# Kernel optimization log

Measured on AMD Instinct MI355X. Metric: run time of the kernel, lower is better.

## Reference

```python
import jax, jax.numpy as jnp
import numpy as np

NUM_NODES = 262144
NUM_GRAPHS = 256
D_MODEL = 256
LOG_2 = float(np.log(2.0))


def setup_inputs() -> dict:
    key = jax.random.key(0)
    k1, k2, k3 = jax.random.split(key, 3)
    l_enc = jax.random.normal(k1, (NUM_NODES, D_MODEL), dtype=jnp.float32)
    g_enc = jax.random.normal(k2, (NUM_GRAPHS, D_MODEL), dtype=jnp.float32)
    batch = jax.random.randint(k3, (NUM_NODES,), 0, NUM_GRAPHS, dtype=jnp.int64)
    return {"l_enc": l_enc, "g_enc": g_enc, "batch": batch}


def reference(l_enc, g_enc, batch):
    # local_global_loss_ with measure='JSD', mask=[] (msk == ones)
    num_nodes = l_enc.shape[0]
    num_graphs = g_enc.shape[0]
    # pos_mask: one-hot of graph id per node; neg_mask is its complement
    pos_mask = jax.nn.one_hot(batch, num_graphs, dtype=l_enc.dtype)  # [N, G]
    neg_mask = 1.0 - pos_mask
    res = jnp.einsum('nd,gd->ng', l_enc, g_enc)                      # [N, G]
    # JSD positive expectation on res*pos_mask (zeros contribute 0)
    Ep = LOG_2 - jax.nn.softplus(-(res * pos_mask))
    # JSD negative expectation on res*neg_mask (zeros contribute 0)
    rq = res * neg_mask
    Eq = jax.nn.softplus(-rq) + rq - LOG_2
    E_pos = jnp.sum(Ep) / num_nodes
    E_neg = jnp.sum(Eq) / (num_nodes * (num_graphs - 1))
    return E_neg - E_pos
```

## Files before the change

### kernel.cpp

```cpp
#include <hip/hip_runtime.h>
#include <hip/hip_bf16.h>

#define N_NODES 262144
#define N_GRAPHS 256
#define DMODEL 256
#define LN2 0.6931471805599453094

typedef __attribute__((ext_vector_type(4))) float f32x4;
typedef __attribute__((ext_vector_type(8))) short short8;

__device__ __forceinline__ short bf(float x) {
    __hip_bfloat16 h = __float2bfloat16(x);
    return __builtin_bit_cast(short, h);
}

__device__ __forceinline__ short8 cvt8(f32x4 lo, f32x4 hi) {
    short8 a;
    a[0] = bf(lo[0]); a[1] = bf(lo[1]); a[2] = bf(lo[2]); a[3] = bf(lo[3]);
    a[4] = bf(hi[0]); a[5] = bf(hi[1]); a[6] = bf(hi[2]); a[7] = bf(hi[3]);
    return a;
}

__device__ __forceinline__ void mfma8(short8 a, const char* bb, f32x4* acc) {
#pragma unroll
    for (int nt = 0; nt < 8; ++nt) {
        short8 bfrag = *reinterpret_cast<const short8*>(bb + nt * 1024);
        acc[nt] = __builtin_amdgcn_mfma_f32_16x16x32_bf16(a, bfrag, acc[nt], 0, 0, 0);
    }
}

__device__ __forceinline__ void elem(float r, int col, int bv,
                                     float& Sl2, float& Sl2p, float& Spr) {
    float t = fminf(r, 64.f) * 1.44269504f;
    float l2 = __log2f(1.f + exp2f(t));
    Sl2 += l2;
    float m = (col == bv) ? 1.f : 0.f;
    Sl2p = fmaf(m, l2, Sl2p);
    Spr = fmaf(m, r, Spr);
}

__global__ __launch_bounds__(256, 1) void mvgrl_main(
    const float* __restrict__ l_enc, const float* __restrict__ g_enc,
    const int* __restrict__ batch, double* __restrict__ partials) {
    extern __shared__ char lds_raw[];

    const int tid = threadIdx.x;
    const int lane = tid & 63;
    const int wave = tid >> 6;
    const int bid = blockIdx.x;

    const int rg = (bid >> 4) * 8 + (bid & 7);
    const int chalf = (bid >> 3) & 1;
    const int row_blk = rg * 1024;
    const int kofs = (lane >> 4) * 8;

    f32x4 s0l, s0h, s1l, s1h, s2l, s2h, s3l, s3h;
    const float* arow = l_enc +
        (size_t)(row_blk + wave * 16 + (lane & 15)) * DMODEL + kofs;
    s0l = *reinterpret_cast<const f32x4*>(arow + 0);
    s0h = *reinterpret_cast<const f32x4*>(arow + 4);
    s1l = *reinterpret_cast<const f32x4*>(arow + 32);
    s1h = *reinterpret_cast<const f32x4*>(arow + 36);
    s2l = *reinterpret_cast<const f32x4*>(arow + 64);
    s2h = *reinterpret_cast<const f32x4*>(arow + 68);
    s3l = *reinterpret_cast<const f32x4*>(arow + 96);
    s3h = *reinterpret_cast<const f32x4*>(arow + 100);

    {
        short8* lb = reinterpret_cast<short8*>(lds_raw);
#pragma unroll 2
        for (int i = 0; i < 16; ++i) {
            int c = wave + i * 4;
            int nt = c & 7, ks = c >> 3;
            int g = chalf * 128 + nt * 16 + (lane & 15);
            int k = ks * 32 + (lane >> 4) * 8;
            const float* src = g_enc + g * DMODEL + k;
            f32x4 lo = *reinterpret_cast<const f32x4*>(src);
            f32x4 hi = *reinterpret_cast<const f32x4*>(src + 4);
            lb[c * 64 + lane] = cvt8(lo, hi);
        }
    }
    __syncthreads();

    const char* ldsB = lds_raw + lane * 16;
    double dS0 = 0.0, dS1 = 0.0, dS2 = 0.0;

#pragma unroll 1
    for (int pass = 0; pass < 16; ++pass) {
        const int rowbase = row_blk + pass * 64 + wave * 16;
        const int rsub = (lane >> 4) * 4;
        int bv0 = batch[rowbase + rsub + 0];
        int bv1 = batch[rowbase + rsub + 1];
        int bv2 = batch[rowbase + rsub + 2];
        int bv3 = batch[rowbase + rsub + 3];

        const float* arow_next = l_enc +
            (size_t)(row_blk + ((pass + 1) & 15) * 64 + wave * 16 + (lane & 15)) *
                DMODEL + kofs;

        f32x4 acc[8];
#pragma unroll
        for (int n = 0; n < 8; ++n) acc[n] = (f32x4){0.f, 0.f, 0.f, 0.f};

#pragma unroll 1
        for (int g = 0; g < 2; ++g) {
            const float* src = (g == 0) ? (arow + 128) : arow_next;
            const char* lb = ldsB + (size_t)g * 4 * 8192;
            {
                short8 a = cvt8(s0l, s0h);
                s0l = *reinterpret_cast<const f32x4*>(src + 0);
                s0h = *reinterpret_cast<const f32x4*>(src + 4);
                mfma8(a, lb + 0 * 8192, acc);
            }
            {
                short8 a = cvt8(s1l, s1h);
                s1l = *reinterpret_cast<const f32x4*>(src + 32);
                s1h = *reinterpret_cast<const f32x4*>(src + 36);
                mfma8(a, lb + 1 * 8192, acc);
            }
            {
                short8 a = cvt8(s2l, s2h);
                s2l = *reinterpret_cast<const f32x4*>(src + 64);
                s2h = *reinterpret_cast<const f32x4*>(src + 68);
                mfma8(a, lb + 2 * 8192, acc);
            }
            {
                short8 a = cvt8(s3l, s3h);
                s3l = *reinterpret_cast<const f32x4*>(src + 96);
                s3h = *reinterpret_cast<const f32x4*>(src + 100);
                mfma8(a, lb + 3 * 8192, acc);
            }
        }
        arow = arow_next;

        float Sl2 = 0.f, Sl2p = 0.f, Spr = 0.f;
        const int colbase = chalf * 128 + (lane & 15);
#pragma unroll
        for (int nt = 0; nt < 8; ++nt) {
            const int col = colbase + nt * 16;
            f32x4 av = acc[nt];
            elem(av[0], col, bv0, Sl2, Sl2p, Spr);
            elem(av[1], col, bv1, Sl2, Sl2p, Spr);
            elem(av[2], col, bv2, Sl2, Sl2p, Spr);
            elem(av[3], col, bv3, Sl2, Sl2p, Spr);
        }
        dS0 += (double)Sl2;
        dS1 += (double)Sl2p;
        dS2 += (double)Spr;
    }

#pragma unroll
    for (int off = 32; off; off >>= 1) {
        dS0 += __shfl_xor(dS0, off);
        dS1 += __shfl_xor(dS1, off);
        dS2 += __shfl_xor(dS2, off);
    }
    __syncthreads();
    double* red = reinterpret_cast<double*>(lds_raw);
    if (lane == 0) {
        red[wave * 3 + 0] = dS0;
        red[wave * 3 + 1] = dS1;
        red[wave * 3 + 2] = dS2;
    }
    __syncthreads();
    if (tid == 0) {
        double a = 0, b = 0, c = 0;
#pragma unroll
        for (int w = 0; w < 4; ++w) {
            a += red[w * 3 + 0];
            b += red[w * 3 + 1];
            c += red[w * 3 + 2];
        }
        partials[bid * 3 + 0] = a;
        partials[bid * 3 + 1] = b;
        partials[bid * 3 + 2] = c;
    }
}

__global__ void finalize_kernel(const double* __restrict__ p,
                                float* __restrict__ out) {
    int t = threadIdx.x;
    double a = p[t * 3 + 0], b = p[t * 3 + 1], c = p[t * 3 + 2];
#pragma unroll
    for (int off = 32; off; off >>= 1) {
        a += __shfl_xor(a, off);
        b += __shfl_xor(b, off);
        c += __shfl_xor(c, off);
    }
    __shared__ double red[24];
    int lane = t & 63, w = t >> 6;
    if (lane == 0) { red[w * 3] = a; red[w * 3 + 1] = b; red[w * 3 + 2] = c; }
    __syncthreads();
    if (t == 0) {
        double A = 0, B = 0, C = 0;
#pragma unroll
        for (int i = 0; i < 8; ++i) {
            A += red[i * 3]; B += red[i * 3 + 1]; C += red[i * 3 + 2];
        }
        const double NN = (double)N_NODES, GG = (double)N_GRAPHS;
        double Sall_q = LN2 * A - NN * GG * LN2;
        double Spq = LN2 * B - NN * LN2;
        double Spr = C;
        double neg = (Sall_q - Spq) / (NN * (GG - 1.0));
        double pos = (Spr - Spq) / NN;
        out[0] = (float)(neg - pos);
    }
}

extern "C" void kernel_launch(void* const* d_in, const int* in_sizes, int n_in,
                              void* d_out, int out_size, void* d_ws,
                              size_t ws_size, hipStream_t stream) {
    const float* l_enc = (const float*)d_in[0];
    const float* g_enc = (const float*)d_in[1];
    const int* batch = (const int*)d_in[2];
    float* out = (float*)d_out;

    double* partials = (double*)d_ws;

    (void)hipFuncSetAttribute(reinterpret_cast<const void*>(mvgrl_main),
                              hipFuncAttributeMaxDynamicSharedMemorySize, 65536);

    mvgrl_main<<<512, 256, 65536, stream>>>(l_enc, g_enc, batch, partials);
    finalize_kernel<<<1, 512, 0, stream>>>(partials, out);
}
```

Measured before the change: 83.86 us.

## Keep g_enc B fragments in registers and double-buffer l_enc rows in LDS

Each wave now keeps its 64-column slice of g_enc (all 256 K) as bf16 fragments in registers. Each block handles 512 rows across all 256 columns, where before two blocks split the columns of each row group. l_enc rows are staged 16 at a time through a padded, double-buffered LDS tile shared by all four waves, so each row is read from global memory once instead of twice. This costs a block-wide barrier every 16 rows, many more live registers (32 short8 B fragments), and narrower per-wave MFMA work per step.

```diff
diff --git a/kernel.cpp b/kernel.cpp
--- a/kernel.cpp
+++ b/kernel.cpp
@@ -5,6 +5,7 @@
 #define N_GRAPHS 256
 #define DMODEL 256
 #define LN2 0.6931471805599453094
+#define ROW_STRIDE 1040
 
 typedef __attribute__((ext_vector_type(4))) float f32x4;
 typedef __attribute__((ext_vector_type(8))) short short8;
@@ -19,14 +20,6 @@
     a[0] = bf(lo[0]); a[1] = bf(lo[1]); a[2] = bf(lo[2]); a[3] = bf(lo[3]);
     a[4] = bf(hi[0]); a[5] = bf(hi[1]); a[6] = bf(hi[2]); a[7] = bf(hi[3]);
     return a;
-}
-
-__device__ __forceinline__ void mfma8(short8 a, const char* bb, f32x4* acc) {
-#pragma unroll
-    for (int nt = 0; nt < 8; ++nt) {
-        short8 bfrag = *reinterpret_cast<const short8*>(bb + nt * 1024);
-        acc[nt] = __builtin_amdgcn_mfma_f32_16x16x32_bf16(a, bfrag, acc[nt], 0, 0, 0);
-    }
 }
 
 __device__ __forceinline__ void elem(float r, int col, int bv,
@@ -48,105 +41,122 @@
     const int lane = tid & 63;
     const int wave = tid >> 6;
     const int bid = blockIdx.x;
-
-    const int rg = (bid >> 4) * 8 + (bid & 7);
-    const int chalf = (bid >> 3) & 1;
-    const int row_blk = rg * 1024;
-    const int kofs = (lane >> 4) * 8;
-
-    f32x4 s0l, s0h, s1l, s1h, s2l, s2h, s3l, s3h;
-    const float* arow = l_enc +
-        (size_t)(row_blk + wave * 16 + (lane & 15)) * DMODEL + kofs;
-    s0l = *reinterpret_cast<const f32x4*>(arow + 0);
-    s0h = *reinterpret_cast<const f32x4*>(arow + 4);
-    s1l = *reinterpret_cast<const f32x4*>(arow + 32);
-    s1h = *reinterpret_cast<const f32x4*>(arow + 36);
-    s2l = *reinterpret_cast<const f32x4*>(arow + 64);
-    s2h = *reinterpret_cast<const f32x4*>(arow + 68);
-    s3l = *reinterpret_cast<const f32x4*>(arow + 96);
-    s3h = *reinterpret_cast<const f32x4*>(arow + 100);
+    const int row_blk = bid * 512;
+
+    short8 b0_0, b0_1, b0_2, b0_3, b1_0, b1_1, b1_2, b1_3;
+    short8 b2_0, b2_1, b2_2, b2_3, b3_0, b3_1, b3_2, b3_3;
+    short8 b4_0, b4_1, b4_2, b4_3, b5_0, b5_1, b5_2, b5_3;
+    short8 b6_0, b6_1, b6_2, b6_3, b7_0, b7_1, b7_2, b7_3;
+#define LOADB(ks, nt) { \
+    const float* s = g_enc + \
+        (size_t)(wave * 64 + nt * 16 + (lane & 15)) * DMODEL + \
+        ks * 32 + (lane >> 4) * 8; \
+    b##ks##_##nt = cvt8(*reinterpret_cast<const f32x4*>(s), \
+                        *reinterpret_cast<const f32x4*>(s + 4)); }
+    LOADB(0,0) LOADB(0,1) LOADB(0,2) LOADB(0,3)
+    LOADB(1,0) LOADB(1,1) LOADB(1,2) LOADB(1,3)
+    LOADB(2,0) LOADB(2,1) LOADB(2,2) LOADB(2,3)
+    LOADB(3,0) LOADB(3,1) LOADB(3,2) LOADB(3,3)
+    LOADB(4,0) LOADB(4,1) LOADB(4,2) LOADB(4,3)
+    LOADB(5,0) LOADB(5,1) LOADB(5,2) LOADB(5,3)
+    LOADB(6,0) LOADB(6,1) LOADB(6,2) LOADB(6,3)
+    LOADB(7,0) LOADB(7,1) LOADB(7,2) LOADB(7,3)
+#undef LOADB
+
+    char* abuf0 = lds_raw;
+    char* abuf1 = lds_raw + 16 * ROW_STRIDE;
 
     {
-        short8* lb = reinterpret_cast<short8*>(lds_raw);
-#pragma unroll 2
-        for (int i = 0; i < 16; ++i) {
-            int c = wave + i * 4;
-            int nt = c & 7, ks = c >> 3;
-            int g = chalf * 128 + nt * 16 + (lane & 15);
-            int k = ks * 32 + (lane >> 4) * 8;
-            const float* src = g_enc + g * DMODEL + k;
-            f32x4 lo = *reinterpret_cast<const f32x4*>(src);
-            f32x4 hi = *reinterpret_cast<const f32x4*>(src + 4);
-            lb[c * 64 + lane] = cvt8(lo, hi);
-        }
+        const float* g = l_enc + (size_t)(row_blk + wave * 4) * DMODEL;
+        f32x4 t0 = *reinterpret_cast<const f32x4*>(g + 0 * DMODEL + lane * 4);
+        f32x4 t1 = *reinterpret_cast<const f32x4*>(g + 1 * DMODEL + lane * 4);
+        f32x4 t2 = *reinterpret_cast<const f32x4*>(g + 2 * DMODEL + lane * 4);
+        f32x4 t3 = *reinterpret_cast<const f32x4*>(g + 3 * DMODEL + lane * 4);
+        *reinterpret_cast<f32x4*>(abuf0 + (wave * 4 + 0) * ROW_STRIDE + lane * 16) = t0;
+        *reinterpret_cast<f32x4*>(abuf0 + (wave * 4 + 1) * ROW_STRIDE + lane * 16) = t1;
+        *reinterpret_cast<f32x4*>(abuf0 + (wave * 4 + 2) * ROW_STRIDE + lane * 16) = t2;
+        *reinterpret_cast<f32x4*>(abuf0 + (wave * 4 + 3) * ROW_STRIDE + lane * 16) = t3;
     }
     __syncthreads();
 
-    const char* ldsB = lds_raw + lane * 16;
     double dS0 = 0.0, dS1 = 0.0, dS2 = 0.0;
 
 #pragma unroll 1
-    for (int pass = 0; pass < 16; ++pass) {
-        const int rowbase = row_blk + pass * 64 + wave * 16;
+    for (int p = 0; p < 32; ++p) {
+        char* acur = (p & 1) ? abuf1 : abuf0;
+        char* anxt = (p & 1) ? abuf0 : abuf1;
+        const int rowbase = row_blk + p * 16;
+
+        const int pn = (p + 1) & 31;
+        const float* g = l_enc + (size_t)(row_blk + pn * 16 + wave * 4) * DMODEL;
+        f32x4 t0 = *reinterpret_cast<const f32x4*>(g + 0 * DMODEL + lane * 4);
+        f32x4 t1 = *reinterpret_cast<const f32x4*>(g + 1 * DMODEL + lane * 4);
+        f32x4 t2 = *reinterpret_cast<const f32x4*>(g + 2 * DMODEL + lane * 4);
+        f32x4 t3 = *reinterpret_cast<const f32x4*>(g + 3 * DMODEL + lane * 4);
+
         const int rsub = (lane >> 4) * 4;
         int bv0 = batch[rowbase + rsub + 0];
         int bv1 = batch[rowbase + rsub + 1];
         int bv2 = batch[rowbase + rsub + 2];
         int bv3 = batch[rowbase + rsub + 3];
 
-        const float* arow_next = l_enc +
-            (size_t)(row_blk + ((pass + 1) & 15) * 64 + wave * 16 + (lane & 15)) *
-                DMODEL + kofs;
-
-        f32x4 acc[8];
-#pragma unroll
-        for (int n = 0; n < 8; ++n) acc[n] = (f32x4){0.f, 0.f, 0.f, 0.f};
-
-#pragma unroll 1
-        for (int g = 0; g < 2; ++g) {
-            const float* src = (g == 0) ? (arow + 128) : arow_next;
-            const char* lb = ldsB + (size_t)g * 4 * 8192;
-            {
-                short8 a = cvt8(s0l, s0h);
-                s0l = *reinterpret_cast<const f32x4*>(src + 0);
-                s0h = *reinterpret_cast<const f32x4*>(src + 4);
-                mfma8(a, lb + 0 * 8192, acc);
-            }
-            {
-                short8 a = cvt8(s1l, s1h);
-                s1l = *reinterpret_cast<const f32x4*>(src + 32);
-                s1h = *reinterpret_cast<const f32x4*>(src + 36);
-                mfma8(a, lb + 1 * 8192, acc);
-            }
-            {
-                short8 a = cvt8(s2l, s2h);
-                s2l = *reinterpret_cast<const f32x4*>(src + 64);
-                s2h = *reinterpret_cast<const f32x4*>(src + 68);
-                mfma8(a, lb + 2 * 8192, acc);
-            }
-            {
-                short8 a = cvt8(s3l, s3h);
-                s3l = *reinterpret_cast<const f32x4*>(src + 96);
-                s3h = *reinterpret_cast<const f32x4*>(src + 100);
-                mfma8(a, lb + 3 * 8192, acc);
-            }
-        }
-        arow = arow_next;
+        f32x4 acc0 = (f32x4){0.f, 0.f, 0.f, 0.f};
+        f32x4 acc1 = (f32x4){0.f, 0.f, 0.f, 0.f};
+        f32x4 acc2 = (f32x4){0.f, 0.f, 0.f, 0.f};
+        f32x4 acc3 = (f32x4){0.f, 0.f, 0.f, 0.f};
+
+        const char* ar = acur + (lane & 15) * ROW_STRIDE + (lane >> 4) * 32;
+#define KSTEP(ks) { \
+        f32x4 alo = *reinterpret_cast<const f32x4*>(ar + ks * 128); \
+        f32x4 ahi = *reinterpret_cast<const f32x4*>(ar + ks * 128 + 16); \
+        short8 a = cvt8(alo, ahi); \
+        acc0 = __builtin_amdgcn_mfma_f32_16x16x32_bf16(a, b##ks##_0, acc0, 0, 0, 0); \
+        acc1 = __builtin_amdgcn_mfma_f32_16x16x32_bf16(a, b##ks##_1, acc1, 0, 0, 0); \
+        acc2 = __builtin_amdgcn_mfma_f32_16x16x32_bf16(a, b##ks##_2, acc2, 0, 0, 0); \
+        acc3 = __builtin_amdgcn_mfma_f32_16x16x32_bf16(a, b##ks##_3, acc3, 0, 0, 0); }
+        KSTEP(0) KSTEP(1) KSTEP(2) KSTEP(3)
+        KSTEP(4) KSTEP(5) KSTEP(6) KSTEP(7)
+#undef KSTEP
 
         float Sl2 = 0.f, Sl2p = 0.f, Spr = 0.f;
-        const int colbase = chalf * 128 + (lane & 15);
-#pragma unroll
-        for (int nt = 0; nt < 8; ++nt) {
-            const int col = colbase + nt * 16;
-            f32x4 av = acc[nt];
-            elem(av[0], col, bv0, Sl2, Sl2p, Spr);
-            elem(av[1], col, bv1, Sl2, Sl2p, Spr);
-            elem(av[2], col, bv2, Sl2, Sl2p, Spr);
-            elem(av[3], col, bv3, Sl2, Sl2p, Spr);
+        const int colbase = wave * 64 + (lane & 15);
+        {
+            const int col = colbase + 0;
+            elem(acc0[0], col, bv0, Sl2, Sl2p, Spr);
+            elem(acc0[1], col, bv1, Sl2, Sl2p, Spr);
+            elem(acc0[2], col, bv2, Sl2, Sl2p, Spr);
+            elem(acc0[3], col, bv3, Sl2, Sl2p, Spr);
+        }
+        {
+            const int col = colbase + 16;
+            elem(acc1[0], col, bv0, Sl2, Sl2p, Spr);
+            elem(acc1[1], col, bv1, Sl2, Sl2p, Spr);
+            elem(acc1[2], col, bv2, Sl2, Sl2p, Spr);
+            elem(acc1[3], col, bv3, Sl2, Sl2p, Spr);
+        }
+        {
+            const int col = colbase + 32;
+            elem(acc2[0], col, bv0, Sl2, Sl2p, Spr);
+            elem(acc2[1], col, bv1, Sl2, Sl2p, Spr);
+            elem(acc2[2], col, bv2, Sl2, Sl2p, Spr);
+            elem(acc2[3], col, bv3, Sl2, Sl2p, Spr);
+        }
+        {
+            const int col = colbase + 48;
+            elem(acc3[0], col, bv0, Sl2, Sl2p, Spr);
+            elem(acc3[1], col, bv1, Sl2, Sl2p, Spr);
+            elem(acc3[2], col, bv2, Sl2, Sl2p, Spr);
+            elem(acc3[3], col, bv3, Sl2, Sl2p, Spr);
         }
         dS0 += (double)Sl2;
         dS1 += (double)Sl2p;
         dS2 += (double)Spr;
+
+        *reinterpret_cast<f32x4*>(anxt + (wave * 4 + 0) * ROW_STRIDE + lane * 16) = t0;
+        *reinterpret_cast<f32x4*>(anxt + (wave * 4 + 1) * ROW_STRIDE + lane * 16) = t1;
+        *reinterpret_cast<f32x4*>(anxt + (wave * 4 + 2) * ROW_STRIDE + lane * 16) = t2;
+        *reinterpret_cast<f32x4*>(anxt + (wave * 4 + 3) * ROW_STRIDE + lane * 16) = t3;
+        __syncthreads();
     }
 
 #pragma unroll
@@ -155,7 +165,6 @@
         dS1 += __shfl_xor(dS1, off);
         dS2 += __shfl_xor(dS2, off);
     }
-    __syncthreads();
     double* red = reinterpret_cast<double*>(lds_raw);
     if (lane == 0) {
         red[wave * 3 + 0] = dS0;
@@ -218,8 +227,8 @@
     double* partials = (double*)d_ws;
 
     (void)hipFuncSetAttribute(reinterpret_cast<const void*>(mvgrl_main),
-                              hipFuncAttributeMaxDynamicSharedMemorySize, 65536);
-
-    mvgrl_main<<<512, 256, 65536, stream>>>(l_enc, g_enc, batch, partials);
+                              hipFuncAttributeMaxDynamicSharedMemorySize, 33280);
+
+    mvgrl_main<<<512, 256, 33280, stream>>>(l_enc, g_enc, batch, partials);
     finalize_kernel<<<1, 512, 0, stream>>>(partials, out);
 }
```

Measured after the change: 124.7 us. 1.49x slower.

## Switch MFMA tiling from 16x16x32 to 32x32x16 bf16 with 32-row wave tiles

Applied to the files above, without the earlier changes.

Replaces the 16x16x32 bf16 MFMA tiling with 32x32x16 instructions. Each wave now computes a 32x128 tile per pass, so the kernel runs half as many passes. The A-fragment loads, LDS layout of g_enc, batch index gather and epilogue mapping are all reworked to match the 32x32 accumulator layout. The aim is fewer LDS B-fragment reads per FLOP and better MFMA efficiency, at the cost of larger accumulators (64 floats per lane) and more batch loads per lane.

```diff
diff --git a/kernel.cpp b/kernel.cpp
--- a/kernel.cpp
+++ b/kernel.cpp
@@ -7,6 +7,7 @@
 #define LN2 0.6931471805599453094
 
 typedef __attribute__((ext_vector_type(4))) float f32x4;
+typedef __attribute__((ext_vector_type(16))) float f32x16;
 typedef __attribute__((ext_vector_type(8))) short short8;
 
 __device__ __forceinline__ short bf(float x) {
@@ -19,14 +20,6 @@
     a[0] = bf(lo[0]); a[1] = bf(lo[1]); a[2] = bf(lo[2]); a[3] = bf(lo[3]);
     a[4] = bf(hi[0]); a[5] = bf(hi[1]); a[6] = bf(hi[2]); a[7] = bf(hi[3]);
     return a;
-}
-
-__device__ __forceinline__ void mfma8(short8 a, const char* bb, f32x4* acc) {
-#pragma unroll
-    for (int nt = 0; nt < 8; ++nt) {
-        short8 bfrag = *reinterpret_cast<const short8*>(bb + nt * 1024);
-        acc[nt] = __builtin_amdgcn_mfma_f32_16x16x32_bf16(a, bfrag, acc[nt], 0, 0, 0);
-    }
 }
 
 __device__ __forceinline__ void elem(float r, int col, int bv,
@@ -52,28 +45,29 @@
     const int rg = (bid >> 4) * 8 + (bid & 7);
     const int chalf = (bid >> 3) & 1;
     const int row_blk = rg * 1024;
-    const int kofs = (lane >> 4) * 8;
+    const int alane = lane & 31;
+    const int aoct = (lane >> 5) * 8;
 
     f32x4 s0l, s0h, s1l, s1h, s2l, s2h, s3l, s3h;
     const float* arow = l_enc +
-        (size_t)(row_blk + wave * 16 + (lane & 15)) * DMODEL + kofs;
+        (size_t)(row_blk + wave * 32 + alane) * DMODEL + aoct;
     s0l = *reinterpret_cast<const f32x4*>(arow + 0);
     s0h = *reinterpret_cast<const f32x4*>(arow + 4);
-    s1l = *reinterpret_cast<const f32x4*>(arow + 32);
-    s1h = *reinterpret_cast<const f32x4*>(arow + 36);
-    s2l = *reinterpret_cast<const f32x4*>(arow + 64);
-    s2h = *reinterpret_cast<const f32x4*>(arow + 68);
-    s3l = *reinterpret_cast<const f32x4*>(arow + 96);
-    s3h = *reinterpret_cast<const f32x4*>(arow + 100);
+    s1l = *reinterpret_cast<const f32x4*>(arow + 16);
+    s1h = *reinterpret_cast<const f32x4*>(arow + 20);
+    s2l = *reinterpret_cast<const f32x4*>(arow + 32);
+    s2h = *reinterpret_cast<const f32x4*>(arow + 36);
+    s3l = *reinterpret_cast<const f32x4*>(arow + 48);
+    s3h = *reinterpret_cast<const f32x4*>(arow + 52);
 
     {
         short8* lb = reinterpret_cast<short8*>(lds_raw);
 #pragma unroll 2
         for (int i = 0; i < 16; ++i) {
             int c = wave + i * 4;
-            int nt = c & 7, ks = c >> 3;
-            int g = chalf * 128 + nt * 16 + (lane & 15);
-            int k = ks * 32 + (lane >> 4) * 8;
+            int nt = c & 3, ks = c >> 2;
+            int g = chalf * 128 + nt * 32 + (lane & 31);
+            int k = ks * 16 + (lane >> 5) * 8;
             const float* src = g_enc + g * DMODEL + k;
             f32x4 lo = *reinterpret_cast<const f32x4*>(src);
             f32x4 hi = *reinterpret_cast<const f32x4*>(src + 4);
@@ -86,64 +80,94 @@
     double dS0 = 0.0, dS1 = 0.0, dS2 = 0.0;
 
 #pragma unroll 1
-    for (int pass = 0; pass < 16; ++pass) {
-        const int rowbase = row_blk + pass * 64 + wave * 16;
-        const int rsub = (lane >> 4) * 4;
-        int bv0 = batch[rowbase + rsub + 0];
-        int bv1 = batch[rowbase + rsub + 1];
-        int bv2 = batch[rowbase + rsub + 2];
-        int bv3 = batch[rowbase + rsub + 3];
+    for (int pass = 0; pass < 8; ++pass) {
+        const int rowbase = row_blk + pass * 128 + wave * 32;
+
+        const int hi4 = (lane >> 5) * 4;
+        int bv[4][4];
+#pragma unroll
+        for (int oct = 0; oct < 4; ++oct)
+#pragma unroll
+            for (int r = 0; r < 4; ++r)
+                bv[oct][r] = batch[rowbase + hi4 + r + 8 * oct];
 
         const float* arow_next = l_enc +
-            (size_t)(row_blk + ((pass + 1) & 15) * 64 + wave * 16 + (lane & 15)) *
-                DMODEL + kofs;
-
-        f32x4 acc[8];
-#pragma unroll
-        for (int n = 0; n < 8; ++n) acc[n] = (f32x4){0.f, 0.f, 0.f, 0.f};
+            (size_t)(row_blk + ((pass + 1) & 7) * 128 + wave * 32 + alane) *
+                DMODEL + aoct;
+
+        f32x16 acc0 = (f32x16)(0.f), acc1 = (f32x16)(0.f);
+        f32x16 acc2 = (f32x16)(0.f), acc3 = (f32x16)(0.f);
 
 #pragma unroll 1
-        for (int g = 0; g < 2; ++g) {
-            const float* src = (g == 0) ? (arow + 128) : arow_next;
-            const char* lb = ldsB + (size_t)g * 4 * 8192;
+        for (int g = 0; g < 4; ++g) {
+            const float* src = (g < 3) ? (arow + 64 * (g + 1)) : arow_next;
+            const char* gb = ldsB + (size_t)g * 16384;
             {
                 short8 a = cvt8(s0l, s0h);
                 s0l = *reinterpret_cast<const f32x4*>(src + 0);
                 s0h = *reinterpret_cast<const f32x4*>(src + 4);
-                mfma8(a, lb + 0 * 8192, acc);
+                acc0 = __builtin_amdgcn_mfma_f32_32x32x16_bf16(a,
+                    *reinterpret_cast<const short8*>(gb + 0 * 1024), acc0, 0, 0, 0);
+                acc1 = __builtin_amdgcn_mfma_f32_32x32x16_bf16(a,
+                    *reinterpret_cast<const short8*>(gb + 1 * 1024), acc1, 0, 0, 0);
+                acc2 = __builtin_amdgcn_mfma_f32_32x32x16_bf16(a,
+                    *reinterpret_cast<const short8*>(gb + 2 * 1024), acc2, 0, 0, 0);
+                acc3 = __builtin_amdgcn_mfma_f32_32x32x16_bf16(a,
+                    *reinterpret_cast<const short8*>(gb + 3 * 1024), acc3, 0, 0, 0);
             }
             {
                 short8 a = cvt8(s1l, s1h);
-                s1l = *reinterpret_cast<const f32x4*>(src + 32);
-                s1h = *reinterpret_cast<const f32x4*>(src + 36);
-                mfma8(a, lb + 1 * 8192, acc);
+                s1l = *reinterpret_cast<const f32x4*>(src + 16);
+                s1h = *reinterpret_cast<const f32x4*>(src + 20);
+                acc0 = __builtin_amdgcn_mfma_f32_32x32x16_bf16(a,
+                    *reinterpret_cast<const short8*>(gb + 4 * 1024), acc0, 0, 0, 0);
+                acc1 = __builtin_amdgcn_mfma_f32_32x32x16_bf16(a,
+                    *reinterpret_cast<const short8*>(gb + 5 * 1024), acc1, 0, 0, 0);
+                acc2 = __builtin_amdgcn_mfma_f32_32x32x16_bf16(a,
+                    *reinterpret_cast<const short8*>(gb + 6 * 1024), acc2, 0, 0, 0);
+                acc3 = __builtin_amdgcn_mfma_f32_32x32x16_bf16(a,
+                    *reinterpret_cast<const short8*>(gb + 7 * 1024), acc3, 0, 0, 0);
             }
             {
                 short8 a = cvt8(s2l, s2h);
-                s2l = *reinterpret_cast<const f32x4*>(src + 64);
-                s2h = *reinterpret_cast<const f32x4*>(src + 68);
-                mfma8(a, lb + 2 * 8192, acc);
+                s2l = *reinterpret_cast<const f32x4*>(src + 32);
+                s2h = *reinterpret_cast<const f32x4*>(src + 36);
+                acc0 = __builtin_amdgcn_mfma_f32_32x32x16_bf16(a,
+                    *reinterpret_cast<const short8*>(gb + 8 * 1024), acc0, 0, 0, 0);
+                acc1 = __builtin_amdgcn_mfma_f32_32x32x16_bf16(a,
+                    *reinterpret_cast<const short8*>(gb + 9 * 1024), acc1, 0, 0, 0);
+                acc2 = __builtin_amdgcn_mfma_f32_32x32x16_bf16(a,
+                    *reinterpret_cast<const short8*>(gb + 10 * 1024), acc2, 0, 0, 0);
+                acc3 = __builtin_amdgcn_mfma_f32_32x32x16_bf16(a,
+                    *reinterpret_cast<const short8*>(gb + 11 * 1024), acc3, 0, 0, 0);
             }
             {
                 short8 a = cvt8(s3l, s3h);
-                s3l = *reinterpret_cast<const f32x4*>(src + 96);
-                s3h = *reinterpret_cast<const f32x4*>(src + 100);
-                mfma8(a, lb + 3 * 8192, acc);
+                s3l = *reinterpret_cast<const f32x4*>(src + 48);
+                s3h = *reinterpret_cast<const f32x4*>(src + 52);
+                acc0 = __builtin_amdgcn_mfma_f32_32x32x16_bf16(a,
+                    *reinterpret_cast<const short8*>(gb + 12 * 1024), acc0, 0, 0, 0);
+                acc1 = __builtin_amdgcn_mfma_f32_32x32x16_bf16(a,
+                    *reinterpret_cast<const short8*>(gb + 13 * 1024), acc1, 0, 0, 0);
+                acc2 = __builtin_amdgcn_mfma_f32_32x32x16_bf16(a,
+                    *reinterpret_cast<const short8*>(gb + 14 * 1024), acc2, 0, 0, 0);
+                acc3 = __builtin_amdgcn_mfma_f32_32x32x16_bf16(a,
+                    *reinterpret_cast<const short8*>(gb + 15 * 1024), acc3, 0, 0, 0);
             }
         }
         arow = arow_next;
 
         float Sl2 = 0.f, Sl2p = 0.f, Spr = 0.f;
-        const int colbase = chalf * 128 + (lane & 15);
-#pragma unroll
-        for (int nt = 0; nt < 8; ++nt) {
-            const int col = colbase + nt * 16;
-            f32x4 av = acc[nt];
-            elem(av[0], col, bv0, Sl2, Sl2p, Spr);
-            elem(av[1], col, bv1, Sl2, Sl2p, Spr);
-            elem(av[2], col, bv2, Sl2, Sl2p, Spr);
-            elem(av[3], col, bv3, Sl2, Sl2p, Spr);
-        }
+        const int colb = chalf * 128 + (lane & 31);
+#define EPI(accv, t)                                                      \
+        {                                                                 \
+            const int col = colb + t * 32;                                \
+            _Pragma("unroll")                                             \
+            for (int r = 0; r < 16; ++r)                                  \
+                elem(accv[r], col, bv[r >> 2][r & 3], Sl2, Sl2p, Spr);    \
+        }
+        EPI(acc0, 0) EPI(acc1, 1) EPI(acc2, 2) EPI(acc3, 3)
+#undef EPI
         dS0 += (double)Sl2;
         dS1 += (double)Sl2p;
         dS2 += (double)Spr;
```

Result: slower. 91.41 us (+9.0%).
